# Kernel optimization log

Measured on AMD Instinct MI355X. Metric: run time of the kernel, lower is better.

The kernel has to match this reference:

```python
import jax, jax.numpy as jnp
import numpy as np

B, T, C, HS = 8, 2048, 2048, 128  # batch, seq, n_embedding, head_size
THETA = 10000.0


def _rope_tables(dim, seq_len, theta=THETA):
    freqs = 1.0 / theta ** (jnp.arange(0, dim, 2, dtype=jnp.float32) / dim)  # [dim/2]
    t = jnp.arange(seq_len, dtype=jnp.float32)
    ang = jnp.outer(t, freqs)  # [T, dim/2]
    return jnp.cos(ang), jnp.sin(ang)


def _apply_rope(v, cos, sin):
    # v: [B,T,D]; pairs along last dim treated as complex (real=even, imag=odd)
    b, t, d = v.shape
    vr = v.reshape(b, t, d // 2, 2)
    x0, x1 = vr[..., 0], vr[..., 1]
    o0 = x0 * cos - x1 * sin
    o1 = x0 * sin + x1 * cos
    return jnp.stack([o0, o1], axis=-1).reshape(b, t, d)


def setup_inputs() -> dict:
    key = jax.random.key(0)
    k1, k2, k3, k4 = jax.random.split(key, 4)
    scale = 1.0 / np.sqrt(C)
    x = jax.random.normal(k1, (B, T, C), dtype=jnp.float32)
    Wk = jax.random.normal(k2, (C, HS), dtype=jnp.float32) * scale
    Wq = jax.random.normal(k3, (C, HS), dtype=jnp.float32) * scale
    Wv = jax.random.normal(k4, (C, HS), dtype=jnp.float32) * scale
    return {"x": x, "Wk": Wk, "Wq": Wq, "Wv": Wv}


def reference(x, Wk, Wq, Wv):
    b, t, _ = x.shape
    cos, sin = _rope_tables(HS, t)
    k = x @ Wk  # [B,T,HS]
    q = x @ Wq
    # Source: xq,xk = apply_rotary_emb(key, query); query,key = xq,xk
    # => scores = rope(q_proj) @ rope(k_proj)^T (standard causal attention)
    qr = _apply_rope(q, cos, sin)
    kr = _apply_rope(k, cos, sin)
    scores = jnp.einsum('btd,bsd->bts', qr, kr) * (HS ** -0.5)  # [B,T,T]
    causal = jnp.tril(jnp.ones((t, t), dtype=bool))
    scores = jnp.where(causal, scores, -jnp.inf)
    wei = jax.nn.softmax(scores, axis=-1)
    v = x @ Wv
    return jnp.einsum('bts,bsd->btd', wei, v)
```

## Files before the change

### kernel.cpp

```cpp
#include <hip/hip_runtime.h>

#define NB 8
#define NT 2048
#define NC 2048
#define NH 128

typedef short s8v __attribute__((ext_vector_type(8)));
typedef float f4  __attribute__((ext_vector_type(4)));

static __device__ __forceinline__ unsigned short f2bf(float f) {
    union { float f; unsigned int u; } v; v.f = f;
    unsigned int x = v.u;
    return (unsigned short)((x + 0x7FFFu + ((x >> 16) & 1u)) >> 16);
}

static __device__ __forceinline__ void gl2lds16(const void* g, void* lds_base) {
    __builtin_amdgcn_global_load_lds(
        (const __attribute__((address_space(1))) unsigned int*)g,
        (__attribute__((address_space(3))) unsigned int*)lds_base, 16, 0, 0);
}

__global__ __launch_bounds__(256) void wtrans_k(
    const float* __restrict__ Wk, const float* __restrict__ Wq,
    const float* __restrict__ Wv, unsigned short* __restrict__ wt)
{
    __shared__ float Ls[64][129];
    const int mat = blockIdx.y;
    const float* W = (mat == 0) ? Wq : (mat == 1) ? Wk : Wv;
    const int k0 = blockIdx.x * 64;
    const int t  = threadIdx.x;

    #pragma unroll
    for (int j = 0; j < 8; ++j) {
        int flat = j * 1024 + t * 4;
        int k = flat >> 7, n = flat & 127;
        f4 v = *reinterpret_cast<const f4*>(W + (size_t)(k0 + k) * NH + n);
        Ls[k][n] = v[0]; Ls[k][n + 1] = v[1]; Ls[k][n + 2] = v[2]; Ls[k][n + 3] = v[3];
    }
    __syncthreads();

    const int n = t >> 1, half = t & 1;
    unsigned short tmp[32];
    #pragma unroll
    for (int kk = 0; kk < 32; ++kk) tmp[kk] = f2bf(Ls[half * 32 + kk][n]);
    unsigned short* dst = wt + (size_t)mat * 262144 + (size_t)n * 2048 + k0 + half * 32;
    #pragma unroll
    for (int v = 0; v < 4; ++v)
        *reinterpret_cast<s8v*>(dst + v * 8) = *reinterpret_cast<s8v*>(tmp + v * 8);
}

__global__ __launch_bounds__(256, 2) void proj_rope(
    const float* __restrict__ x, const unsigned short* __restrict__ wt,
    unsigned short* __restrict__ qws, unsigned short* __restrict__ kws,
    unsigned short* __restrict__ vtws)
{
    __shared__ char LDS[57344];
    char* XsB = LDS;
    char* BsB = LDS + 8192;

    const int wave = threadIdx.x >> 6;
    const int lane = threadIdx.x & 63;
    const int quad = lane >> 4, l16 = lane & 15;
    const int M0 = blockIdx.x * 32;

    const float* xbase[2];
    #pragma unroll
    for (int s = 0; s < 2; ++s) {
        const int xrow = wave * 8 + s * 4 + (lane >> 4);
        const int xcol = ((lane & 15) ^ (xrow & 15)) * 4;
        xbase[s] = x + (size_t)(M0 + xrow) * NC + xcol;
    }
    const unsigned short* bbase[12];
    const int bc = (lane & 7) ^ (lane >> 3);
    #pragma unroll
    for (int s = 0; s < 12; ++s) {
        const int brow = wave * 96 + s * 8 + (lane >> 3);
        bbase[s] = wt + (size_t)brow * NC + bc * 8;
    }

    f4 acc[2][6];
    #pragma unroll
    for (int mi = 0; mi < 2; ++mi)
        #pragma unroll
        for (int ni = 0; ni < 6; ++ni)
            acc[mi][ni] = (f4){0.f, 0.f, 0.f, 0.f};

    for (int kk = 0; kk < NC; kk += 64) {
        #pragma unroll
        for (int s = 0; s < 2; ++s)
            gl2lds16(xbase[s] + kk, XsB + (wave * 2 + s) * 1024);
        #pragma unroll
        for (int s = 0; s < 12; ++s)
            gl2lds16(bbase[s] + kk, BsB + (wave * 12 + s) * 1024);
        __syncthreads();

        #pragma unroll
        for (int ksub = 0; ksub < 2; ++ksub) {
            s8v a[2];
            #pragma unroll
            for (int mi = 0; mi < 2; ++mi) {
                const int rb = (mi * 16 + l16) * 256;
                const int p0 = (ksub * 8 + quad * 2) ^ l16;
                union { f4 f; unsigned int u[4]; } L, H;
                L.f = *reinterpret_cast<const f4*>(XsB + rb + p0 * 16);
                H.f = *reinterpret_cast<const f4*>(XsB + rb + (p0 ^ 1) * 16);
                union { s8v s; unsigned int u[4]; } A;
                A.u[0] = __builtin_amdgcn_perm(L.u[1], L.u[0], 0x07060302u);
                A.u[1] = __builtin_amdgcn_perm(L.u[3], L.u[2], 0x07060302u);
                A.u[2] = __builtin_amdgcn_perm(H.u[1], H.u[0], 0x07060302u);
                A.u[3] = __builtin_amdgcn_perm(H.u[3], H.u[2], 0x07060302u);
                a[mi] = A.s;
            }
            #pragma unroll
            for (int ni = 0; ni < 6; ++ni) {
                const int row2 = wave * 96 + ni * 16 + l16;
                const int pb = (ksub * 4 + quad) ^ (l16 & 7);
                s8v b = *reinterpret_cast<const s8v*>(BsB + row2 * 128 + pb * 16);
                acc[0][ni] = __builtin_amdgcn_mfma_f32_16x16x32_bf16(a[0], b, acc[0][ni], 0, 0, 0);
                acc[1][ni] = __builtin_amdgcn_mfma_f32_16x16x32_bf16(a[1], b, acc[1][ni], 0, 0, 0);
            }
        }
        __syncthreads();
    }

    const float cfreq = -0.10381025296f;
    #pragma unroll
    for (int mi = 0; mi < 2; ++mi) {
        #pragma unroll
        for (int ni = 0; ni < 6; ++ni) {
            const int outcol = wave * 96 + ni * 16 + l16;
            const int mat = outcol >> 7;
            const int col = outcol & 127;
            #pragma unroll
            for (int r = 0; r < 4; ++r) {
                const int row = M0 + mi * 16 + quad * 4 + r;
                const int t   = row & (NT - 1);
                float v = acc[mi][ni][r];
                if (mat < 2) {
                    float other = __shfl_xor(v, 1, 64);
                    float freq  = exp2f(cfreq * (float)(col & ~1));
                    float ang   = (float)t * freq;
                    float sn = sinf(ang), cs = cosf(ang);
                    v = (col & 1) ? (other * sn + v * cs)
                                  : (v * cs - other * sn);
                }
                unsigned short bv = f2bf(v);
                if (mat == 0)      qws[(size_t)row * NH + col] = bv;
                else if (mat == 1) kws[(size_t)row * NH + col] = bv;
                else {
                    int b = row >> 11;
                    vtws[(size_t)b * (NH * NT) + (size_t)col * NT + t] = bv;
                }
            }
        }
    }
}

__global__ __launch_bounds__(256, 2) void attn_k(
    const unsigned short* __restrict__ qws, const unsigned short* __restrict__ kws,
    const unsigned short* __restrict__ vtws, float* __restrict__ out)
{
    __shared__ unsigned short P[4][32 * 64];
    __shared__ float Os[4][32][64];
    __shared__ float Ms[4][32], Ls[4][32], Lt[32];

    const int wave = threadIdx.x >> 6;
    const int lane = threadIdx.x & 63;
    const int quad = lane >> 4, l16 = lane & 15;
    const int b     = blockIdx.y;
    const int qrow0 = blockIdx.x * 32;
    const unsigned short* Q  = qws  + (size_t)b * NT * NH;
    const unsigned short* K  = kws  + (size_t)b * NT * NH;
    const unsigned short* Vt = vtws + (size_t)b * NH * NT;

    s8v qf[2][4];
    #pragma unroll
    for (int mi = 0; mi < 2; ++mi)
        #pragma unroll
        for (int ks = 0; ks < 4; ++ks)
            qf[mi][ks] = *reinterpret_cast<const s8v*>(
                Q + (size_t)(qrow0 + mi * 16 + l16) * NH + ks * 32 + quad * 8);

    float m[2][4], ls[2][4];
    f4 o[2][8];
    #pragma unroll
    for (int mi = 0; mi < 2; ++mi) {
        #pragma unroll
        for (int r = 0; r < 4; ++r) { m[mi][r] = -INFINITY; ls[mi][r] = 0.f; }
        #pragma unroll
        for (int dt = 0; dt < 8; ++dt) o[mi][dt] = (f4){0.f, 0.f, 0.f, 0.f};
    }

    const int nkt = (qrow0 >> 6) + 1;
    const float scale2 = 0.1275166948f;

    for (int kt = wave; kt < nkt; kt += 4) {
        const int kbase = kt * 64;
        const bool domask = (kt == nkt - 1);

        f4 s[2][4];
        #pragma unroll
        for (int nt = 0; nt < 4; ++nt) {
            f4 a0 = (f4){0.f, 0.f, 0.f, 0.f}, a1 = a0;
            #pragma unroll
            for (int ks = 0; ks < 4; ++ks) {
                s8v kf = *reinterpret_cast<const s8v*>(
                    K + (size_t)(kbase + nt * 16 + l16) * NH + ks * 32 + quad * 8);
                a0 = __builtin_amdgcn_mfma_f32_16x16x32_bf16(qf[0][ks], kf, a0, 0, 0, 0);
                a1 = __builtin_amdgcn_mfma_f32_16x16x32_bf16(qf[1][ks], kf, a1, 0, 0, 0);
            }
            s[0][nt] = a0; s[1][nt] = a1;
        }

        float tmx[2][4];
        #pragma unroll
        for (int mi = 0; mi < 2; ++mi) {
            #pragma unroll
            for (int r = 0; r < 4; ++r) {
                const int trow = qrow0 + mi * 16 + quad * 4 + r;
                #pragma unroll
                for (int nt = 0; nt < 4; ++nt) {
                    float sv = s[mi][nt][r] * scale2;
                    if (domask && (kbase + nt * 16 + l16 > trow)) sv = -INFINITY;
                    s[mi][nt][r] = sv;
                }
                float tm = fmaxf(fmaxf(s[mi][0][r], s[mi][1][r]),
                                 fmaxf(s[mi][2][r], s[mi][3][r]));
                #pragma unroll
                for (int off = 1; off < 16; off <<= 1)
                    tm = fmaxf(tm, __shfl_xor(tm, off, 64));
                tmx[mi][r] = tm;
            }
        }

        bool grow = false;
        #pragma unroll
        for (int mi = 0; mi < 2; ++mi)
            #pragma unroll
            for (int r = 0; r < 4; ++r)
                grow = grow || (tmx[mi][r] > m[mi][r] + 8.0f);
        if (__any(grow)) {
            #pragma unroll
            for (int mi = 0; mi < 2; ++mi)
                #pragma unroll
                for (int r = 0; r < 4; ++r) {
                    const float mn = fmaxf(m[mi][r], tmx[mi][r]);
                    const float alpha = exp2f(m[mi][r] - mn);
                    m[mi][r] = mn;
                    ls[mi][r] *= alpha;
                    #pragma unroll
                    for (int dt = 0; dt < 8; ++dt) o[mi][dt][r] *= alpha;
                }
        }

        #pragma unroll
        for (int mi = 0; mi < 2; ++mi)
            #pragma unroll
            for (int r = 0; r < 4; ++r) {
                float rs = 0.f;
                #pragma unroll
                for (int nt = 0; nt < 4; ++nt) {
                    float p = exp2f(s[mi][nt][r] - m[mi][r]);
                    s[mi][nt][r] = p;
                    rs += p;
                }
                ls[mi][r] += rs;
            }

        #pragma unroll
        for (int mi = 0; mi < 2; ++mi)
            #pragma unroll
            for (int nt = 0; nt < 4; ++nt)
                #pragma unroll
                for (int r = 0; r < 4; ++r) {
                    const int prow = mi * 16 + quad * 4 + r;
                    const int swz  = ((nt * 2 + (l16 >> 3)) ^ (prow & 7)) * 8 + (l16 & 7);
                    P[wave][prow * 64 + swz] = f2bf(s[mi][nt][r]);
                }

        #pragma unroll
        for (int ks2 = 0; ks2 < 2; ++ks2) {
            s8v pa[2];
            #pragma unroll
            for (int mi = 0; mi < 2; ++mi) {
                const int prow = mi * 16 + l16;
                const int pp = ((ks2 * 4 + quad) ^ (l16 & 7));
                pa[mi] = *reinterpret_cast<const s8v*>(&P[wave][prow * 64 + pp * 8]);
            }
            #pragma unroll
            for (int dt = 0; dt < 8; ++dt) {
                s8v vf = *reinterpret_cast<const s8v*>(
                    Vt + (size_t)(dt * 16 + l16) * NT + kbase + ks2 * 32 + quad * 8);
                o[0][dt] = __builtin_amdgcn_mfma_f32_16x16x32_bf16(pa[0], vf, o[0][dt], 0, 0, 0);
                o[1][dt] = __builtin_amdgcn_mfma_f32_16x16x32_bf16(pa[1], vf, o[1][dt], 0, 0, 0);
            }
        }
    }

    #pragma unroll
    for (int mi = 0; mi < 2; ++mi)
        #pragma unroll
        for (int r = 0; r < 4; ++r) {
            float v = ls[mi][r];
            #pragma unroll
            for (int off = 1; off < 16; off <<= 1) v += __shfl_xor(v, off, 64);
            ls[mi][r] = v;
        }

    if (l16 == 0) {
        #pragma unroll
        for (int mi = 0; mi < 2; ++mi)
            #pragma unroll
            for (int r = 0; r < 4; ++r) {
                Ms[wave][mi * 16 + quad * 4 + r] = m[mi][r];
                Ls[wave][mi * 16 + quad * 4 + r] = ls[mi][r];
            }
    }
    __syncthreads();

    #pragma unroll
    for (int mi = 0; mi < 2; ++mi)
        #pragma unroll
        for (int r = 0; r < 4; ++r) {
            const int row = mi * 16 + quad * 4 + r;
            float M = fmaxf(fmaxf(Ms[0][row], Ms[1][row]), fmaxf(Ms[2][row], Ms[3][row]));
            float sc = exp2f(m[mi][r] - M);
            float lt = Ls[0][row] * exp2f(Ms[0][row] - M) + Ls[1][row] * exp2f(Ms[1][row] - M)
                     + Ls[2][row] * exp2f(Ms[2][row] - M) + Ls[3][row] * exp2f(Ms[3][row] - M);
            if (wave == 0 && l16 == 0) Lt[row] = lt;
            #pragma unroll
            for (int dt = 0; dt < 8; ++dt) o[mi][dt][r] *= sc;
        }

    const int rrow = threadIdx.x >> 3;
    const int cx   = (threadIdx.x & 7) * 8;
    #pragma unroll
    for (int h = 0; h < 2; ++h) {
        __syncthreads();
        #pragma unroll
        for (int mi = 0; mi < 2; ++mi)
            #pragma unroll
            for (int dtl = 0; dtl < 4; ++dtl)
                #pragma unroll
                for (int r = 0; r < 4; ++r)
                    Os[wave][mi * 16 + quad * 4 + r][dtl * 16 + l16] = o[mi][h * 4 + dtl][r];
        __syncthreads();
        f4 s0 = (f4){0.f, 0.f, 0.f, 0.f}, s1 = s0;
        #pragma unroll
        for (int w = 0; w < 4; ++w) {
            s0 += *reinterpret_cast<const f4*>(&Os[w][rrow][cx]);
            s1 += *reinterpret_cast<const f4*>(&Os[w][rrow][cx + 4]);
        }
        const float rl = 1.0f / Lt[rrow];
        float* dst = &out[((size_t)b * NT + qrow0 + rrow) * NH + h * 64 + cx];
        *reinterpret_cast<f4*>(dst)     = s0 * rl;
        *reinterpret_cast<f4*>(dst + 4) = s1 * rl;
    }
}

extern "C" void kernel_launch(void* const* d_in, const int* in_sizes, int n_in,
                              void* d_out, int out_size, void* d_ws, size_t ws_size,
                              hipStream_t stream) {
    const float* x  = (const float*)d_in[0];
    const float* Wk = (const float*)d_in[1];
    const float* Wq = (const float*)d_in[2];
    const float* Wv = (const float*)d_in[3];
    unsigned short* ws   = (unsigned short*)d_ws;
    unsigned short* wt   = ws;
    unsigned short* qws  = ws  + 786432;
    unsigned short* kws  = qws + 2097152;
    unsigned short* vtws = kws + 2097152;
    float* outp = (float*)d_out;

    wtrans_k<<<dim3(32, 3), 256, 0, stream>>>(Wk, Wq, Wv, wt);
    proj_rope<<<dim3(512), 256, 0, stream>>>(x, wt, qws, kws, vtws);
    attn_k<<<dim3(64, 8), 256, 0, stream>>>(qws, kws, vtws, outp);
}
```

Measured before the change: 321.8 us.

## Load projection GEMM operands directly from global memory instead of LDS staging

The QKV projection GEMM no longer stages x and the transposed weights through LDS with global_load_lds and block barriers. Each wave now loads its MFMA fragments straight from global memory into registers, with a k-step of 32 unrolled by four. This removes the LDS round trip and the __syncthreads stalls, but x rows are no longer shared across the block's four waves. Each wave therefore reads x redundantly, and global access is less coalesced. The launch-bounds occupancy hint is also dropped.

After: 413.5 us. 1.29x slower.

```diff
diff --git a/kernel.cpp b/kernel.cpp
--- a/kernel.cpp
+++ b/kernel.cpp
@@ -12,12 +12,6 @@
     union { float f; unsigned int u; } v; v.f = f;
     unsigned int x = v.u;
     return (unsigned short)((x + 0x7FFFu + ((x >> 16) & 1u)) >> 16);
-}
-
-static __device__ __forceinline__ void gl2lds16(const void* g, void* lds_base) {
-    __builtin_amdgcn_global_load_lds(
-        (const __attribute__((address_space(1))) unsigned int*)g,
-        (__attribute__((address_space(3))) unsigned int*)lds_base, 16, 0, 0);
 }
 
 __global__ __launch_bounds__(256) void wtrans_k(
@@ -49,34 +43,24 @@
         *reinterpret_cast<s8v*>(dst + v * 8) = *reinterpret_cast<s8v*>(tmp + v * 8);
 }
 
-__global__ __launch_bounds__(256, 2) void proj_rope(
+__global__ __launch_bounds__(256) void proj_rope(
     const float* __restrict__ x, const unsigned short* __restrict__ wt,
     unsigned short* __restrict__ qws, unsigned short* __restrict__ kws,
     unsigned short* __restrict__ vtws)
 {
-    __shared__ char LDS[57344];
-    char* XsB = LDS;
-    char* BsB = LDS + 8192;
-
     const int wave = threadIdx.x >> 6;
     const int lane = threadIdx.x & 63;
     const int quad = lane >> 4, l16 = lane & 15;
     const int M0 = blockIdx.x * 32;
 
-    const float* xbase[2];
-    #pragma unroll
-    for (int s = 0; s < 2; ++s) {
-        const int xrow = wave * 8 + s * 4 + (lane >> 4);
-        const int xcol = ((lane & 15) ^ (xrow & 15)) * 4;
-        xbase[s] = x + (size_t)(M0 + xrow) * NC + xcol;
-    }
-    const unsigned short* bbase[12];
-    const int bc = (lane & 7) ^ (lane >> 3);
-    #pragma unroll
-    for (int s = 0; s < 12; ++s) {
-        const int brow = wave * 96 + s * 8 + (lane >> 3);
-        bbase[s] = wt + (size_t)brow * NC + bc * 8;
-    }
+    const float* xb[2];
+    #pragma unroll
+    for (int mi = 0; mi < 2; ++mi)
+        xb[mi] = x + (size_t)(M0 + mi * 16 + l16) * NC + quad * 8;
+    const unsigned short* bb[6];
+    #pragma unroll
+    for (int ni = 0; ni < 6; ++ni)
+        bb[ni] = wt + (size_t)(wave * 96 + ni * 16 + l16) * NC + quad * 8;
 
     f4 acc[2][6];
     #pragma unroll
@@ -85,42 +69,27 @@
         for (int ni = 0; ni < 6; ++ni)
             acc[mi][ni] = (f4){0.f, 0.f, 0.f, 0.f};
 
-    for (int kk = 0; kk < NC; kk += 64) {
-        #pragma unroll
-        for (int s = 0; s < 2; ++s)
-            gl2lds16(xbase[s] + kk, XsB + (wave * 2 + s) * 1024);
-        #pragma unroll
-        for (int s = 0; s < 12; ++s)
-            gl2lds16(bbase[s] + kk, BsB + (wave * 12 + s) * 1024);
-        __syncthreads();
-
-        #pragma unroll
-        for (int ksub = 0; ksub < 2; ++ksub) {
-            s8v a[2];
-            #pragma unroll
-            for (int mi = 0; mi < 2; ++mi) {
-                const int rb = (mi * 16 + l16) * 256;
-                const int p0 = (ksub * 8 + quad * 2) ^ l16;
-                union { f4 f; unsigned int u[4]; } L, H;
-                L.f = *reinterpret_cast<const f4*>(XsB + rb + p0 * 16);
-                H.f = *reinterpret_cast<const f4*>(XsB + rb + (p0 ^ 1) * 16);
-                union { s8v s; unsigned int u[4]; } A;
-                A.u[0] = __builtin_amdgcn_perm(L.u[1], L.u[0], 0x07060302u);
-                A.u[1] = __builtin_amdgcn_perm(L.u[3], L.u[2], 0x07060302u);
-                A.u[2] = __builtin_amdgcn_perm(H.u[1], H.u[0], 0x07060302u);
-                A.u[3] = __builtin_amdgcn_perm(H.u[3], H.u[2], 0x07060302u);
-                a[mi] = A.s;
-            }
-            #pragma unroll
-            for (int ni = 0; ni < 6; ++ni) {
-                const int row2 = wave * 96 + ni * 16 + l16;
-                const int pb = (ksub * 4 + quad) ^ (l16 & 7);
-                s8v b = *reinterpret_cast<const s8v*>(BsB + row2 * 128 + pb * 16);
-                acc[0][ni] = __builtin_amdgcn_mfma_f32_16x16x32_bf16(a[0], b, acc[0][ni], 0, 0, 0);
-                acc[1][ni] = __builtin_amdgcn_mfma_f32_16x16x32_bf16(a[1], b, acc[1][ni], 0, 0, 0);
-            }
-        }
-        __syncthreads();
+    #pragma unroll 4
+    for (int kk = 0; kk < NC; kk += 32) {
+        s8v a[2];
+        #pragma unroll
+        for (int mi = 0; mi < 2; ++mi) {
+            union { f4 f; unsigned int u[4]; } L, H;
+            L.f = *reinterpret_cast<const f4*>(xb[mi] + kk);
+            H.f = *reinterpret_cast<const f4*>(xb[mi] + kk + 4);
+            union { s8v s; unsigned int u[4]; } A;
+            A.u[0] = __builtin_amdgcn_perm(L.u[1], L.u[0], 0x07060302u);
+            A.u[1] = __builtin_amdgcn_perm(L.u[3], L.u[2], 0x07060302u);
+            A.u[2] = __builtin_amdgcn_perm(H.u[1], H.u[0], 0x07060302u);
+            A.u[3] = __builtin_amdgcn_perm(H.u[3], H.u[2], 0x07060302u);
+            a[mi] = A.s;
+        }
+        #pragma unroll
+        for (int ni = 0; ni < 6; ++ni) {
+            s8v b = *reinterpret_cast<const s8v*>(bb[ni] + kk);
+            acc[0][ni] = __builtin_amdgcn_mfma_f32_16x16x32_bf16(a[0], b, acc[0][ni], 0, 0, 0);
+            acc[1][ni] = __builtin_amdgcn_mfma_f32_16x16x32_bf16(a[1], b, acc[1][ni], 0, 0, 0);
+        }
     }
 
     const float cfreq = -0.10381025296f;
```

## Pre-tile weights into MFMA fragment layout and stream B directly from global

Applied to the files above, without the earlier changes.

The weight-transpose kernel now writes bf16 weights in per-fragment 16x32 tile order, so the projection kernel can load B operands straight from global/L2 into registers instead of staging them in LDS. The projection tile grows from 32 to 64 rows, halving the grid to 256 blocks and doubling B reuse per load. x tiles are now double-buffered in LDS, overlapping the next load with the MFMAs. In exchange there are fewer blocks, and each B load now hits L2 latency directly without LDS staging.

Result: slower. 408.1 us (+26.8%).

```diff
diff --git a/kernel.cpp b/kernel.cpp
--- a/kernel.cpp
+++ b/kernel.cpp
@@ -43,67 +43,70 @@
     unsigned short tmp[32];
     #pragma unroll
     for (int kk = 0; kk < 32; ++kk) tmp[kk] = f2bf(Ls[half * 32 + kk][n]);
-    unsigned short* dst = wt + (size_t)mat * 262144 + (size_t)n * 2048 + k0 + half * 32;
+
+    const int nb  = mat * 8 + (n >> 4);
+    const int l16 = n & 15;
+    const int kbi = blockIdx.x * 2 + half;
+    unsigned short* dst = wt + ((size_t)nb * 64 + kbi) * 512;
     #pragma unroll
     for (int v = 0; v < 4; ++v)
-        *reinterpret_cast<s8v*>(dst + v * 8) = *reinterpret_cast<s8v*>(tmp + v * 8);
-}
-
-__global__ __launch_bounds__(256, 2) void proj_rope(
+        *reinterpret_cast<s8v*>(dst + (v * 16 + l16) * 8) = *reinterpret_cast<s8v*>(tmp + v * 8);
+}
+
+__global__ __launch_bounds__(256) void proj_rope(
     const float* __restrict__ x, const unsigned short* __restrict__ wt,
     unsigned short* __restrict__ qws, unsigned short* __restrict__ kws,
     unsigned short* __restrict__ vtws)
 {
-    __shared__ char LDS[57344];
-    char* XsB = LDS;
-    char* BsB = LDS + 8192;
+    __shared__ char LDS[32768];
 
     const int wave = threadIdx.x >> 6;
     const int lane = threadIdx.x & 63;
     const int quad = lane >> 4, l16 = lane & 15;
-    const int M0 = blockIdx.x * 32;
-
-    const float* xbase[2];
-    #pragma unroll
-    for (int s = 0; s < 2; ++s) {
-        const int xrow = wave * 8 + s * 4 + (lane >> 4);
+    const int M0 = blockIdx.x * 64;
+
+    const float* xbase[4];
+    #pragma unroll
+    for (int s = 0; s < 4; ++s) {
+        const int xrow = wave * 16 + s * 4 + (lane >> 4);
         const int xcol = ((lane & 15) ^ (xrow & 15)) * 4;
         xbase[s] = x + (size_t)(M0 + xrow) * NC + xcol;
     }
-    const unsigned short* bbase[12];
-    const int bc = (lane & 7) ^ (lane >> 3);
-    #pragma unroll
-    for (int s = 0; s < 12; ++s) {
-        const int brow = wave * 96 + s * 8 + (lane >> 3);
-        bbase[s] = wt + (size_t)brow * NC + bc * 8;
-    }
-
-    f4 acc[2][6];
-    #pragma unroll
-    for (int mi = 0; mi < 2; ++mi)
+    const unsigned short* bb[6];
+    #pragma unroll
+    for (int ni = 0; ni < 6; ++ni)
+        bb[ni] = wt + ((size_t)(wave * 6 + ni) * 64) * 512 + lane * 8;
+
+    f4 acc[4][6];
+    #pragma unroll
+    for (int mi = 0; mi < 4; ++mi)
         #pragma unroll
         for (int ni = 0; ni < 6; ++ni)
             acc[mi][ni] = (f4){0.f, 0.f, 0.f, 0.f};
 
-    for (int kk = 0; kk < NC; kk += 64) {
-        #pragma unroll
-        for (int s = 0; s < 2; ++s)
-            gl2lds16(xbase[s] + kk, XsB + (wave * 2 + s) * 1024);
-        #pragma unroll
-        for (int s = 0; s < 12; ++s)
-            gl2lds16(bbase[s] + kk, BsB + (wave * 12 + s) * 1024);
-        __syncthreads();
-
+    #pragma unroll
+    for (int s = 0; s < 4; ++s)
+        gl2lds16(xbase[s], LDS + (wave * 4 + s) * 1024);
+    __syncthreads();
+
+    for (int t = 0; t < 32; ++t) {
+        char* Xs = LDS + (t & 1) * 16384;
+        if (t < 31) {
+            char* dstb = LDS + ((t + 1) & 1) * 16384;
+            #pragma unroll
+            for (int s = 0; s < 4; ++s)
+                gl2lds16(xbase[s] + (t + 1) * 64, dstb + (wave * 4 + s) * 1024);
+        }
         #pragma unroll
         for (int ksub = 0; ksub < 2; ++ksub) {
-            s8v a[2];
-            #pragma unroll
-            for (int mi = 0; mi < 2; ++mi) {
+            s8v a[4];
+            #pragma unroll
+            for (int mi = 0; mi < 4; ++mi) {
                 const int rb = (mi * 16 + l16) * 256;
                 const int p0 = (ksub * 8 + quad * 2) ^ l16;
                 union { f4 f; unsigned int u[4]; } L, H;
-                L.f = *reinterpret_cast<const f4*>(XsB + rb + p0 * 16);
-                H.f = *reinterpret_cast<const f4*>(XsB + rb + (p0 ^ 1) * 16);
+                L.f = *reinterpret_cast<const f4*>(Xs + rb + p0 * 16);
+                H.f = *reinterpret_cast<const f4*>(Xs + rb + (p0 ^ 1) * 16);
                 union { s8v s; unsigned int u[4]; } A;
                 A.u[0] = __builtin_amdgcn_perm(L.u[1], L.u[0], 0x07060302u);
                 A.u[1] = __builtin_amdgcn_perm(L.u[3], L.u[2], 0x07060302u);
@@ -111,13 +114,13 @@
                 A.u[3] = __builtin_amdgcn_perm(H.u[3], H.u[2], 0x07060302u);
                 a[mi] = A.s;
             }
+            const int kb = t * 2 + ksub;
             #pragma unroll
             for (int ni = 0; ni < 6; ++ni) {
-                const int row2 = wave * 96 + ni * 16 + l16;
-                const int pb = (ksub * 4 + quad) ^ (l16 & 7);
-                s8v b = *reinterpret_cast<const s8v*>(BsB + row2 * 128 + pb * 16);
-                acc[0][ni] = __builtin_amdgcn_mfma_f32_16x16x32_bf16(a[0], b, acc[0][ni], 0, 0, 0);
-                acc[1][ni] = __builtin_amdgcn_mfma_f32_16x16x32_bf16(a[1], b, acc[1][ni], 0, 0, 0);
+                s8v b = *reinterpret_cast<const s8v*>(bb[ni] + (size_t)kb * 512);
+                #pragma unroll
+                for (int mi = 0; mi < 4; ++mi)
+                    acc[mi][ni] = __builtin_amdgcn_mfma_f32_16x16x32_bf16(a[mi], b, acc[mi][ni], 0, 0, 0);
             }
         }
         __syncthreads();
@@ -125,7 +128,7 @@
 
     const float cfreq = -0.10381025296f;
     #pragma unroll
-    for (int mi = 0; mi < 2; ++mi) {
+    for (int mi = 0; mi < 4; ++mi) {
         #pragma unroll
         for (int ni = 0; ni < 6; ++ni) {
             const int outcol = wave * 96 + ni * 16 + l16;
@@ -373,6 +376,6 @@
     float* outp = (float*)d_out;
 
     wtrans_k<<<dim3(32, 3), 256, 0, stream>>>(Wk, Wq, Wv, wt);
-    proj_rope<<<dim3(512), 256, 0, stream>>>(x, wt, qws, kws, vtws);
+    proj_rope<<<dim3(256), 256, 0, stream>>>(x, wt, qws, kws, vtws);
     attn_k<<<dim3(64, 8), 256, 0, stream>>>(qws, kws, vtws, outp);
 }
```
